# Performance work log

Hardware: AMD Instinct MI355X
Metric: run time of the kernel (lower is better)

## Reference

```python
import jax, jax.numpy as jnp
import numpy as np

B, N, FH, H, FO = 8, 1024, 128, 8, 64
FIN = 2 * FH  # f_hid * 2
NEG = -1e9
SLOPE = 0.2  # leaky_relu negative slope (GAT default)


def setup_inputs() -> dict:
    key = jax.random.key(0)
    ks = jax.random.split(key, 10)
    x = jax.random.normal(ks[0], (B, FIN), jnp.float32)
    A = jax.random.randint(ks[1], (B, N, N), 0, 2, jnp.int32)  # 0/1 dense adjacency
    mask_zero = jnp.ones((B, N, 1), jnp.float32)  # node validity mask
    p_atten = jax.random.uniform(ks[2], (B, N), jnp.float32)  # unused in forward body
    e_atten = jax.random.uniform(ks[3], (B, N, FIN), jnp.float32)
    Npost = jax.random.normal(ks[4], (N, FIN), jnp.float32) * np.float32(1.0 / np.sqrt(FIN))  # kaiming-ish
    w = jax.random.normal(ks[5], (H, FIN, FO), jnp.float32) * np.float32(1.0 / np.sqrt(FIN))
    a_src = jax.random.normal(ks[6], (H, FO), jnp.float32) * np.float32(0.1)
    a_dst = jax.random.normal(ks[7], (H, FO), jnp.float32) * np.float32(0.1)
    bias = jnp.zeros((FO,), jnp.float32)
    return {"x": x, "A": A, "mask_zero": mask_zero, "p_atten": p_atten,
            "e_atten": e_atten, "Npost": Npost, "w": w, "a_src": a_src,
            "a_dst": a_dst, "bias": bias}


def reference(x, A, mask_zero, p_atten, e_atten, Npost, w, a_src, a_dst, bias):
    # broadcast-mul feature gating: x [B,FIN] repeated over N posts, gated by Npost*e_atten
    recx = x[:, None, :] * (Npost[None, :, :] * e_atten)          # [B,N,FIN]
    # BatchGAT (DeepInf-style multi-head graph attention, dropout disabled / eval mode)
    h = jnp.einsum('bnf,hfo->bhno', recx, w)                      # [B,H,N,FO]
    s = jnp.einsum('bhno,ho->bhn', h, a_src)                      # src attention term
    d = jnp.einsum('bhno,ho->bhn', h, a_dst)                      # dst attention term
    logits = jax.nn.leaky_relu(s[:, :, :, None] + d[:, :, None, :], SLOPE)  # [B,H,N,N]
    adj = (A > 0)[:, None, :, :]                                  # [B,1,N,N]
    logits = jnp.where(adj, logits, NEG)
    attn = jax.nn.softmax(logits, axis=-1)                        # masked row softmax
    out = jnp.einsum('bhnm,bhmo->bhno', attn, h) + bias           # aggregate neighbors
    out = out.mean(axis=1)                                        # average heads -> [B,N,FO]
    return out * mask_zero                                        # zero padded nodes
```

## Files before the change

kernel.cpp:

```cpp
#include <hip/hip_runtime.h>

typedef __attribute__((ext_vector_type(8))) short          bf16x8;
typedef __attribute__((ext_vector_type(8))) unsigned short u16x8;
typedef __attribute__((ext_vector_type(4))) unsigned short u16x4;
typedef __attribute__((ext_vector_type(4))) float          f32x4;
typedef __attribute__((ext_vector_type(4))) unsigned int   u32x4;

union U8 { u16x8 u; bf16x8 b; u32x4 w; };
union U4 { u16x4 u; unsigned w[2]; };

__device__ __forceinline__ unsigned short f2bf(float f){
  unsigned u = __float_as_uint(f);
  return (unsigned short)((u + 0x7fffu + ((u >> 16) & 1u)) >> 16);
}
__device__ __forceinline__ unsigned pack_bf16(float lo, float hi){
  unsigned a = __float_as_uint(hi) + 0x8000u;
  unsigned b = __float_as_uint(lo) + 0x8000u;
  return __builtin_amdgcn_perm(a, b, 0x07060302u);
}

#define NN  1024
#define FIN 256
#define NH  8
#define FO  64

__global__ __launch_bounds__(256) void stage0(
    const float* __restrict__ w, const int* __restrict__ A,
    unsigned short* __restrict__ wfrag, unsigned long long* __restrict__ Abits)
{
  const int tid = blockIdx.x * 256 + threadIdx.x;
  if (tid < 16384){
    const int lane = tid & 63, ss = (tid >> 6) & 3, kc = (tid >> 8) & 7, h = tid >> 11;
    const int o = 16 * ss + (lane & 15);
    const int f = kc * 32 + (lane >> 4) * 8;
    u16x8 r;
    #pragma unroll
    for (int j = 0; j < 8; j++) r[j] = f2bf(w[(h * FIN + f + j) * FO + o]);
    *(u16x8*)(wfrag + tid * 8) = r;
  }
  for (int i = tid; i < 8388608; i += 262144){
    unsigned long long m = __ballot(A[i] > 0);
    if ((threadIdx.x & 63) == 0) Abits[i >> 6] = m;
  }
}

__global__ __launch_bounds__(512, 4) void stageA(
    const float* __restrict__ x, const float* __restrict__ e_at,
    const float* __restrict__ Np, const unsigned short* __restrict__ wfrag,
    const float* __restrict__ a_src, const float* __restrict__ a_dst,
    unsigned short* __restrict__ hT,
    float* __restrict__ exps, float* __restrict__ exps2,
    float* __restrict__ expd, float* __restrict__ expd2)
{
  __shared__ unsigned short rex[32 * 264];
  const int t = threadIdx.x;
  const int n0 = blockIdx.x * 32, b = blockIdx.y;

  {
    const int row = t >> 4, f0 = (t & 15) * 16;
    const int nrow = n0 + row;
    const float* ep = e_at + (b * NN + nrow) * FIN + f0;
    const float* qp = Np + nrow * FIN + f0;
    const float* xp = x + b * FIN + f0;
    #pragma unroll
    for (int g = 0; g < 2; g++){
      f32x4 e0 = *(const f32x4*)(ep + g * 8), e1 = *(const f32x4*)(ep + g * 8 + 4);
      f32x4 q0 = *(const f32x4*)(qp + g * 8), q1 = *(const f32x4*)(qp + g * 8 + 4);
      f32x4 x0 = *(const f32x4*)(xp + g * 8), x1 = *(const f32x4*)(xp + g * 8 + 4);
      u16x8 r;
      #pragma unroll
      for (int j = 0; j < 4; j++){
        r[j]     = f2bf(e0[j] * q0[j] * x0[j]);
        r[j + 4] = f2bf(e1[j] * q1[j] * x1[j]);
      }
      *(u16x8*)(rex + row * 264 + f0 + g * 8) = r;
    }
  }
  __syncthreads();

  const int h = t >> 6, lane = t & 63, quad = lane >> 4, l15 = lane & 15;
  const unsigned short* wf = wfrag + h * 16384 + lane * 8;

  f32x4 acc[2][4] = {};
  #pragma unroll
  for (int kc = 0; kc < 8; kc++){
    U8 a0, a1, bf[4];
    a0.u = *(const u16x8*)(rex + l15 * 264 + kc * 32 + quad * 8);
    a1.u = *(const u16x8*)(rex + (16 + l15) * 264 + kc * 32 + quad * 8);
    #pragma unroll
    for (int ss = 0; ss < 4; ss++) bf[ss].u = *(const u16x8*)(wf + (kc * 4 + ss) * 512);
    #pragma unroll
    for (int ss = 0; ss < 4; ss++)
      acc[0][ss] = __builtin_amdgcn_mfma_f32_16x16x32_bf16(a0.b, bf[ss].b, acc[0][ss], 0, 0, 0);
    #pragma unroll
    for (int ss = 0; ss < 4; ss++)
      acc[1][ss] = __builtin_amdgcn_mfma_f32_16x16x32_bf16(a1.b, bf[ss].b, acc[1][ss], 0, 0, 0);
  }

  {
    unsigned short* pan = hT + (size_t)(((b * NH + h) * 32 + (n0 >> 5)) * 64) * 32;
    #pragma unroll
    for (int rg = 0; rg < 2; rg++)
      #pragma unroll
      for (int ss = 0; ss < 4; ss++){
        U4 v;
        v.w[0] = pack_bf16(acc[rg][ss][0], acc[rg][ss][1]);
        v.w[1] = pack_bf16(acc[rg][ss][2], acc[rg][ss][3]);
        *(u16x4*)(pan + (16 * ss + l15) * 32 + rg * 16 + quad * 4) = v.u;
      }
  }

  float as4[4], ad4[4];
  #pragma unroll
  for (int ss = 0; ss < 4; ss++){
    as4[ss] = a_src[h * FO + 16 * ss + l15];
    ad4[ss] = a_dst[h * FO + 16 * ss + l15];
  }
  #pragma unroll
  for (int rg = 0; rg < 2; rg++)
    #pragma unroll
    for (int i = 0; i < 4; i++){
      float ps = 0.f, pd = 0.f;
      #pragma unroll
      for (int ss = 0; ss < 4; ss++){ ps += acc[rg][ss][i] * as4[ss]; pd += acc[rg][ss][i] * ad4[ss]; }
      #pragma unroll
      for (int off = 1; off < 16; off <<= 1){
        ps += __shfl_xor(ps, off);
        pd += __shfl_xor(pd, off);
      }
      if (l15 == 0){
        const int idx = (b * NH + h) * NN + n0 + rg * 16 + quad * 4 + i;
        exps [idx] = __expf(ps);
        exps2[idx] = __expf(0.2f * ps);
        expd [idx] = __expf(pd);
        expd2[idx] = __expf(0.2f * pd);
      }
    }
}

#define PCHUNK(C, PAN)                                                          \
  {                                                                             \
    const int c_ = (C);                                                         \
    const unsigned w0_ = mask_l[l15 * 33 + c_];                                 \
    const unsigned w1_ = mask_l[(16 + l15) * 33 + c_];                          \
    const unsigned ab0_ = w0_ >> (quad * 8), ab1_ = w1_ >> (quad * 8);          \
    f32x4 d0_ = *(const f32x4*)(edh + c_ * 32);                                 \
    f32x4 d1_ = *(const f32x4*)(edh + c_ * 32 + 4);                             \
    f32x4 g0_ = *(const f32x4*)(e2h + c_ * 32);                                 \
    f32x4 g1_ = *(const f32x4*)(e2h + c_ * 32 + 4);                             \
    U8 p0_, p1_;                                                                \
    _Pragma("unroll")                                                           \
    for (int r_ = 0; r_ < 4; r_++){                                             \
      const int j0_ = 2 * r_, j1_ = 2 * r_ + 1;                                 \
      const float dj0_ = (j0_ < 4) ? d0_[j0_] : d1_[j0_ - 4];                   \
      const float gj0_ = (j0_ < 4) ? g0_[j0_] : g1_[j0_ - 4];                   \
      const float dj1_ = (j1_ < 4) ? d0_[j1_] : d1_[j1_ - 4];                   \
      const float gj1_ = (j1_ < 4) ? g0_[j1_] : g1_[j1_ - 4];                   \
      float e00_ = fmaxf(Es0 * dj0_, Es20 * gj0_);                              \
      float e01_ = fmaxf(Es0 * dj1_, Es20 * gj1_);                              \
      float e10_ = fmaxf(Es1 * dj0_, Es21 * gj0_);                              \
      float e11_ = fmaxf(Es1 * dj1_, Es21 * gj1_);                              \
      e00_ = (ab0_ & (1u << j0_)) ? e00_ : 0.f;                                 \
      e01_ = (ab0_ & (1u << j1_)) ? e01_ : 0.f;                                 \
      e10_ = (ab1_ & (1u << j0_)) ? e10_ : 0.f;                                 \
      e11_ = (ab1_ & (1u << j1_)) ? e11_ : 0.f;                                 \
      p0_.w[r_] = pack_bf16(e00_, e01_);                                        \
      p1_.w[r_] = pack_bf16(e10_, e11_);                                        \
    }                                                                           \
    _Pragma("unroll")                                                           \
    for (int ss_ = 0; ss_ < 4; ss_++)                                           \
      acc[0][ss_] = __builtin_amdgcn_mfma_f32_16x16x32_bf16(p0_.b, PAN[ss_].b, acc[0][ss_], 0, 0, 0); \
    accs[0] = __builtin_amdgcn_mfma_f32_16x16x32_bf16(p0_.b, ones.b, accs[0], 0, 0, 0); \
    _Pragma("unroll")                                                           \
    for (int ss_ = 0; ss_ < 4; ss_++)                                           \
      acc[1][ss_] = __builtin_amdgcn_mfma_f32_16x16x32_bf16(p1_.b, PAN[ss_].b, acc[1][ss_], 0, 0, 0); \
    accs[1] = __builtin_amdgcn_mfma_f32_16x16x32_bf16(p1_.b, ones.b, accs[1], 0, 0, 0); \
  }

__global__ __launch_bounds__(1024, 4) void stageB(
    const unsigned* __restrict__ Aw,
    const unsigned short* __restrict__ hT,
    const float* __restrict__ exps, const float* __restrict__ exps2,
    const float* __restrict__ expd, const float* __restrict__ expd2,
    const float* __restrict__ bias, const float* __restrict__ mz,
    float* __restrict__ out)
{
  __shared__ float ed_l[NH * NN];
  __shared__ float e2_l[NH * NN];
  __shared__ unsigned mask_l[32 * 33];
  __shared__ float l_l[NH * 32];
  __shared__ float oacc[32 * 65];
  const int t = threadIdx.x, b = blockIdx.y, n0 = blockIdx.x * 32;
  const int h = (t >> 6) & 7, mh = t >> 9;
  const int lane = t & 63, quad = lane >> 4, l15 = lane & 15;

  for (int i = t; i < 32 * 65; i += 1024) oacc[i] = 0.f;
  if (t < NH * 32) l_l[t] = 0.f;
  {
    const float* s1 = expd  + b * 8192;
    const float* s2 = expd2 + b * 8192;
    *(f32x4*)(ed_l + t * 4)        = *(const f32x4*)(s1 + t * 4);
    *(f32x4*)(ed_l + t * 4 + 4096) = *(const f32x4*)(s1 + t * 4 + 4096);
    *(f32x4*)(e2_l + t * 4)        = *(const f32x4*)(s2 + t * 4);
    *(f32x4*)(e2_l + t * 4 + 4096) = *(const f32x4*)(s2 + t * 4 + 4096);
  }
  mask_l[(t >> 5) * 33 + (t & 31)] = Aw[(b * NN + n0 + (t >> 5)) * 32 + (t & 31)];
  __syncthreads();

  const int hb = (b * NH + h) * NN;
  const float Es0  = exps [hb + n0 + l15],      Es20 = exps2[hb + n0 + l15];
  const float Es1  = exps [hb + n0 + 16 + l15], Es21 = exps2[hb + n0 + 16 + l15];
  const unsigned short* pb = hT + (size_t)(b * NH + h) * 65536 + l15 * 32 + quad * 8;
  const float* edh = ed_l + h * NN + quad * 8;
  const float* e2h = e2_l + h * NN + quad * 8;
  const int c0 = mh * 16;

  U8 ones;
  #pragma unroll
  for (int j = 0; j < 8; j++) ones.u[j] = 0x3F80;

  U8 pan0[4], pan1[4];
  #pragma unroll
  for (int ss = 0; ss < 4; ss++){
    pan0[ss].u = *(const u16x8*)(pb + (size_t)c0 * 2048 + ss * 512);
    pan1[ss].u = *(const u16x8*)(pb + (size_t)(c0 + 1) * 2048 + ss * 512);
  }

  f32x4 acc[2][4] = {};
  f32x4 accs[2] = {};

  for (int cc = 0; cc < 16; cc += 2){
    PCHUNK(c0 + cc, pan0)
    if (cc + 2 < 16){
      #pragma unroll
      for (int ss = 0; ss < 4; ss++)
        pan0[ss].u = *(const u16x8*)(pb + (size_t)(c0 + cc + 2) * 2048 + ss * 512);
    }
    PCHUNK(c0 + cc + 1, pan1)
    if (cc + 3 < 16){
      #pragma unroll
      for (int ss = 0; ss < 4; ss++)
        pan1[ss].u = *(const u16x8*)(pb + (size_t)(c0 + cc + 3) * 2048 + ss * 512);
    }
  }

  if (l15 == 0){
    #pragma unroll
    for (int rg = 0; rg < 2; rg++)
      #pragma unroll
      for (int i = 0; i < 4; i++)
        atomicAdd(&l_l[h * 32 + rg * 16 + quad * 4 + i], accs[rg][i]);
  }
  __syncthreads();

  #pragma unroll
  for (int rg = 0; rg < 2; rg++){
    float inv[4];
    #pragma unroll
    for (int i = 0; i < 4; i++)
      inv[i] = 0.125f / l_l[h * 32 + rg * 16 + quad * 4 + i];
    #pragma unroll
    for (int ss = 0; ss < 4; ss++)
      #pragma unroll
      for (int i = 0; i < 4; i++)
        atomicAdd(&oacc[(rg * 16 + quad * 4 + i) * 65 + ss * 16 + l15], acc[rg][ss][i] * inv[i]);
  }
  __syncthreads();

  for (int i = t; i < 2048; i += 1024){
    const int r = i >> 6, o = i & 63;
    out[(b * NN + n0 + r) * FO + o] = (oacc[r * 65 + o] + bias[o]) * mz[b * NN + n0 + r];
  }
}

extern "C" void kernel_launch(void* const* d_in, const int* in_sizes, int n_in,
                              void* d_out, int out_size, void* d_ws, size_t ws_size,
                              hipStream_t stream)
{
  (void)in_sizes; (void)n_in; (void)out_size; (void)ws_size;
  const float* x    = (const float*)d_in[0];
  const int*   A    = (const int*)d_in[1];
  const float* mz   = (const float*)d_in[2];
  const float* e_at = (const float*)d_in[4];
  const float* Np   = (const float*)d_in[5];
  const float* w    = (const float*)d_in[6];
  const float* asrc = (const float*)d_in[7];
  const float* adst = (const float*)d_in[8];
  const float* bias = (const float*)d_in[9];
  float* out = (float*)d_out;

  char* ws = (char*)d_ws;
  unsigned short* wfrag = (unsigned short*)ws;
  unsigned short* hT    = (unsigned short*)(ws + 262144);
  float* exps  = (float*)(ws + 8650752);
  float* exps2 = (float*)(ws + 8912896);
  float* expd  = (float*)(ws + 9175040);
  float* expd2 = (float*)(ws + 9437184);
  unsigned long long* Abits = (unsigned long long*)(ws + 9699328);

  stage0<<<dim3(1024), dim3(256), 0, stream>>>(w, A, wfrag, Abits);
  stageA<<<dim3(32, 8), dim3(512), 0, stream>>>(x, e_at, Np, wfrag, asrc, adst,
                                                hT, exps, exps2, expd, expd2);
  stageB<<<dim3(32, 8), dim3(1024), 0, stream>>>((const unsigned*)Abits, hT,
                                                 exps, exps2, expd, expd2,
                                                 bias, mz, out);
}
```

Baseline: 177.6 us.

## Split attention stage across head pairs and use global atomics for output

```diff
diff --git a/kernel.cpp b/kernel.cpp
--- a/kernel.cpp
+++ b/kernel.cpp
@@ -26,7 +26,9 @@
 
 __global__ __launch_bounds__(256) void stage0(
     const float* __restrict__ w, const int* __restrict__ A,
-    unsigned short* __restrict__ wfrag, unsigned long long* __restrict__ Abits)
+    const float* __restrict__ bias, const float* __restrict__ mz,
+    unsigned short* __restrict__ wfrag, unsigned long long* __restrict__ Abits,
+    float* __restrict__ out)
 {
   const int tid = blockIdx.x * 256 + threadIdx.x;
   if (tid < 16384){
@@ -37,6 +39,11 @@
     #pragma unroll
     for (int j = 0; j < 8; j++) r[j] = f2bf(w[(h * FIN + f + j) * FO + o]);
     *(u16x8*)(wfrag + tid * 8) = r;
+  }
+  #pragma unroll
+  for (int k = 0; k < 2; k++){
+    const int i = tid + k * 262144;
+    out[i] = bias[i & 63] * mz[i >> 6];
   }
   for (int i = tid; i < 8388608; i += 262144){
     unsigned long long m = __ballot(A[i] > 0);
@@ -52,62 +59,54 @@
     float* __restrict__ exps, float* __restrict__ exps2,
     float* __restrict__ expd, float* __restrict__ expd2)
 {
-  __shared__ unsigned short rex[32 * 264];
+  __shared__ unsigned short rex[16 * 264];
   const int t = threadIdx.x;
-  const int n0 = blockIdx.x * 32, b = blockIdx.y;
+  const int n0 = blockIdx.x * 16, b = blockIdx.y;
 
   {
-    const int row = t >> 4, f0 = (t & 15) * 16;
+    const int row = t >> 5, f0 = (t & 31) * 8;
     const int nrow = n0 + row;
     const float* ep = e_at + (b * NN + nrow) * FIN + f0;
     const float* qp = Np + nrow * FIN + f0;
     const float* xp = x + b * FIN + f0;
-    #pragma unroll
-    for (int g = 0; g < 2; g++){
-      f32x4 e0 = *(const f32x4*)(ep + g * 8), e1 = *(const f32x4*)(ep + g * 8 + 4);
-      f32x4 q0 = *(const f32x4*)(qp + g * 8), q1 = *(const f32x4*)(qp + g * 8 + 4);
-      f32x4 x0 = *(const f32x4*)(xp + g * 8), x1 = *(const f32x4*)(xp + g * 8 + 4);
-      u16x8 r;
-      #pragma unroll
-      for (int j = 0; j < 4; j++){
-        r[j]     = f2bf(e0[j] * q0[j] * x0[j]);
-        r[j + 4] = f2bf(e1[j] * q1[j] * x1[j]);
-      }
-      *(u16x8*)(rex + row * 264 + f0 + g * 8) = r;
-    }
+    f32x4 e0 = *(const f32x4*)ep, e1 = *(const f32x4*)(ep + 4);
+    f32x4 q0 = *(const f32x4*)qp, q1 = *(const f32x4*)(qp + 4);
+    f32x4 x0 = *(const f32x4*)xp, x1 = *(const f32x4*)(xp + 4);
+    u16x8 r;
+    #pragma unroll
+    for (int j = 0; j < 4; j++){
+      r[j]     = f2bf(e0[j] * q0[j] * x0[j]);
+      r[j + 4] = f2bf(e1[j] * q1[j] * x1[j]);
+    }
+    *(u16x8*)(rex + row * 264 + f0) = r;
   }
   __syncthreads();
 
   const int h = t >> 6, lane = t & 63, quad = lane >> 4, l15 = lane & 15;
   const unsigned short* wf = wfrag + h * 16384 + lane * 8;
 
-  f32x4 acc[2][4] = {};
+  f32x4 acc[4] = {};
   #pragma unroll
   for (int kc = 0; kc < 8; kc++){
-    U8 a0, a1, bf[4];
+    U8 a0, bf[4];
     a0.u = *(const u16x8*)(rex + l15 * 264 + kc * 32 + quad * 8);
-    a1.u = *(const u16x8*)(rex + (16 + l15) * 264 + kc * 32 + quad * 8);
     #pragma unroll
     for (int ss = 0; ss < 4; ss++) bf[ss].u = *(const u16x8*)(wf + (kc * 4 + ss) * 512);
     #pragma unroll
     for (int ss = 0; ss < 4; ss++)
-      acc[0][ss] = __builtin_amdgcn_mfma_f32_16x16x32_bf16(a0.b, bf[ss].b, acc[0][ss], 0, 0, 0);
-    #pragma unroll
-    for (int ss = 0; ss < 4; ss++)
-      acc[1][ss] = __builtin_amdgcn_mfma_f32_16x16x32_bf16(a1.b, bf[ss].b, acc[1][ss], 0, 0, 0);
+      acc[ss] = __builtin_amdgcn_mfma_f32_16x16x32_bf16(a0.b, bf[ss].b, acc[ss], 0, 0, 0);
   }
 
   {
-    unsigned short* pan = hT + (size_t)(((b * NH + h) * 32 + (n0 >> 5)) * 64) * 32;
-    #pragma unroll
-    for (int rg = 0; rg < 2; rg++)
-      #pragma unroll
-      for (int ss = 0; ss < 4; ss++){
-        U4 v;
-        v.w[0] = pack_bf16(acc[rg][ss][0], acc[rg][ss][1]);
-        v.w[1] = pack_bf16(acc[rg][ss][2], acc[rg][ss][3]);
-        *(u16x4*)(pan + (16 * ss + l15) * 32 + rg * 16 + quad * 4) = v.u;
-      }
+    const int mtile = blockIdx.x >> 1, moff = (blockIdx.x & 1) * 16;
+    unsigned short* pan = hT + (size_t)(((b * NH + h) * 32 + mtile) * 64) * 32;
+    #pragma unroll
+    for (int ss = 0; ss < 4; ss++){
+      U4 v;
+      v.w[0] = pack_bf16(acc[ss][0], acc[ss][1]);
+      v.w[1] = pack_bf16(acc[ss][2], acc[ss][3]);
+      *(u16x4*)(pan + (16 * ss + l15) * 32 + moff + quad * 4) = v.u;
+    }
   }
 
   float as4[4], ad4[4];
@@ -117,159 +116,115 @@
     ad4[ss] = a_dst[h * FO + 16 * ss + l15];
   }
   #pragma unroll
-  for (int rg = 0; rg < 2; rg++)
-    #pragma unroll
-    for (int i = 0; i < 4; i++){
-      float ps = 0.f, pd = 0.f;
-      #pragma unroll
-      for (int ss = 0; ss < 4; ss++){ ps += acc[rg][ss][i] * as4[ss]; pd += acc[rg][ss][i] * ad4[ss]; }
-      #pragma unroll
-      for (int off = 1; off < 16; off <<= 1){
-        ps += __shfl_xor(ps, off);
-        pd += __shfl_xor(pd, off);
-      }
-      if (l15 == 0){
-        const int idx = (b * NH + h) * NN + n0 + rg * 16 + quad * 4 + i;
-        exps [idx] = __expf(ps);
-        exps2[idx] = __expf(0.2f * ps);
-        expd [idx] = __expf(pd);
-        expd2[idx] = __expf(0.2f * pd);
-      }
-    }
-}
-
-#define PCHUNK(C, PAN)                                                          \
-  {                                                                             \
-    const int c_ = (C);                                                         \
-    const unsigned w0_ = mask_l[l15 * 33 + c_];                                 \
-    const unsigned w1_ = mask_l[(16 + l15) * 33 + c_];                          \
-    const unsigned ab0_ = w0_ >> (quad * 8), ab1_ = w1_ >> (quad * 8);          \
-    f32x4 d0_ = *(const f32x4*)(edh + c_ * 32);                                 \
-    f32x4 d1_ = *(const f32x4*)(edh + c_ * 32 + 4);                             \
-    f32x4 g0_ = *(const f32x4*)(e2h + c_ * 32);                                 \
-    f32x4 g1_ = *(const f32x4*)(e2h + c_ * 32 + 4);                             \
-    U8 p0_, p1_;                                                                \
-    _Pragma("unroll")                                                           \
-    for (int r_ = 0; r_ < 4; r_++){                                             \
-      const int j0_ = 2 * r_, j1_ = 2 * r_ + 1;                                 \
-      const float dj0_ = (j0_ < 4) ? d0_[j0_] : d1_[j0_ - 4];                   \
-      const float gj0_ = (j0_ < 4) ? g0_[j0_] : g1_[j0_ - 4];                   \
-      const float dj1_ = (j1_ < 4) ? d0_[j1_] : d1_[j1_ - 4];                   \
-      const float gj1_ = (j1_ < 4) ? g0_[j1_] : g1_[j1_ - 4];                   \
-      float e00_ = fmaxf(Es0 * dj0_, Es20 * gj0_);                              \
-      float e01_ = fmaxf(Es0 * dj1_, Es20 * gj1_);                              \
-      float e10_ = fmaxf(Es1 * dj0_, Es21 * gj0_);                              \
-      float e11_ = fmaxf(Es1 * dj1_, Es21 * gj1_);                              \
-      e00_ = (ab0_ & (1u << j0_)) ? e00_ : 0.f;                                 \
-      e01_ = (ab0_ & (1u << j1_)) ? e01_ : 0.f;                                 \
-      e10_ = (ab1_ & (1u << j0_)) ? e10_ : 0.f;                                 \
-      e11_ = (ab1_ & (1u << j1_)) ? e11_ : 0.f;                                 \
-      p0_.w[r_] = pack_bf16(e00_, e01_);                                        \
-      p1_.w[r_] = pack_bf16(e10_, e11_);                                        \
-    }                                                                           \
-    _Pragma("unroll")                                                           \
-    for (int ss_ = 0; ss_ < 4; ss_++)                                           \
-      acc[0][ss_] = __builtin_amdgcn_mfma_f32_16x16x32_bf16(p0_.b, PAN[ss_].b, acc[0][ss_], 0, 0, 0); \
-    accs[0] = __builtin_amdgcn_mfma_f32_16x16x32_bf16(p0_.b, ones.b, accs[0], 0, 0, 0); \
-    _Pragma("unroll")                                                           \
-    for (int ss_ = 0; ss_ < 4; ss_++)                                           \
-      acc[1][ss_] = __builtin_amdgcn_mfma_f32_16x16x32_bf16(p1_.b, PAN[ss_].b, acc[1][ss_], 0, 0, 0); \
-    accs[1] = __builtin_amdgcn_mfma_f32_16x16x32_bf16(p1_.b, ones.b, accs[1], 0, 0, 0); \
-  }
-
-__global__ __launch_bounds__(1024, 4) void stageB(
+  for (int i = 0; i < 4; i++){
+    float ps = 0.f, pd = 0.f;
+    #pragma unroll
+    for (int ss = 0; ss < 4; ss++){ ps += acc[ss][i] * as4[ss]; pd += acc[ss][i] * ad4[ss]; }
+    #pragma unroll
+    for (int off = 1; off < 16; off <<= 1){
+      ps += __shfl_xor(ps, off);
+      pd += __shfl_xor(pd, off);
+    }
+    if (l15 == 0){
+      const int idx = (b * NH + h) * NN + n0 + quad * 4 + i;
+      exps [idx] = __expf(ps);
+      exps2[idx] = __expf(0.2f * ps);
+      expd [idx] = __expf(pd);
+      expd2[idx] = __expf(0.2f * pd);
+    }
+  }
+}
+
+__global__ __launch_bounds__(512, 8) void stageB(
     const unsigned* __restrict__ Aw,
     const unsigned short* __restrict__ hT,
     const float* __restrict__ exps, const float* __restrict__ exps2,
     const float* __restrict__ expd, const float* __restrict__ expd2,
-    const float* __restrict__ bias, const float* __restrict__ mz,
-    float* __restrict__ out)
-{
-  __shared__ float ed_l[NH * NN];
-  __shared__ float e2_l[NH * NN];
+    const float* __restrict__ mz, float* __restrict__ out)
+{
+  __shared__ float ed_l[2 * NN];
+  __shared__ float e2_l[2 * NN];
   __shared__ unsigned mask_l[32 * 33];
-  __shared__ float l_l[NH * 32];
-  __shared__ float oacc[32 * 65];
-  const int t = threadIdx.x, b = blockIdx.y, n0 = blockIdx.x * 32;
-  const int h = (t >> 6) & 7, mh = t >> 9;
-  const int lane = t & 63, quad = lane >> 4, l15 = lane & 15;
-
-  for (int i = t; i < 32 * 65; i += 1024) oacc[i] = 0.f;
-  if (t < NH * 32) l_l[t] = 0.f;
+  __shared__ float l_l[4 * 16];
+  const int t = threadIdx.x;
+  const int n0 = blockIdx.x * 32, hq = blockIdx.y, b = blockIdx.z;
+  const int w = t >> 6, lane = t & 63, quad = lane >> 4, l15 = lane & 15;
+  const int hl = w & 1, rg = (w >> 1) & 1, mh = w >> 2;
+  const int h = hq * 2 + hl;
+
+  if (t < 64) l_l[t] = 0.f;
   {
-    const float* s1 = expd  + b * 8192;
-    const float* s2 = expd2 + b * 8192;
-    *(f32x4*)(ed_l + t * 4)        = *(const f32x4*)(s1 + t * 4);
-    *(f32x4*)(ed_l + t * 4 + 4096) = *(const f32x4*)(s1 + t * 4 + 4096);
-    *(f32x4*)(e2_l + t * 4)        = *(const f32x4*)(s2 + t * 4);
-    *(f32x4*)(e2_l + t * 4 + 4096) = *(const f32x4*)(s2 + t * 4 + 4096);
-  }
-  mask_l[(t >> 5) * 33 + (t & 31)] = Aw[(b * NN + n0 + (t >> 5)) * 32 + (t & 31)];
+    const float* s1 = expd  + (b * NH + hq * 2) * NN;
+    const float* s2 = expd2 + (b * NH + hq * 2) * NN;
+    *(f32x4*)(ed_l + t * 4) = *(const f32x4*)(s1 + t * 4);
+    *(f32x4*)(e2_l + t * 4) = *(const f32x4*)(s2 + t * 4);
+  }
+  #pragma unroll
+  for (int k = 0; k < 2; k++){
+    const int i = t + k * 512;
+    mask_l[(i >> 5) * 33 + (i & 31)] = Aw[(b * NN + n0 + (i >> 5)) * 32 + (i & 31)];
+  }
   __syncthreads();
 
   const int hb = (b * NH + h) * NN;
-  const float Es0  = exps [hb + n0 + l15],      Es20 = exps2[hb + n0 + l15];
-  const float Es1  = exps [hb + n0 + 16 + l15], Es21 = exps2[hb + n0 + 16 + l15];
+  const float Es  = exps [hb + n0 + rg * 16 + l15];
+  const float Es2 = exps2[hb + n0 + rg * 16 + l15];
   const unsigned short* pb = hT + (size_t)(b * NH + h) * 65536 + l15 * 32 + quad * 8;
-  const float* edh = ed_l + h * NN + quad * 8;
-  const float* e2h = e2_l + h * NN + quad * 8;
+  const float* edh = ed_l + hl * NN + quad * 8;
+  const float* e2h = e2_l + hl * NN + quad * 8;
+  const unsigned* maskp = mask_l + (rg * 16 + l15) * 33;
   const int c0 = mh * 16;
 
-  U8 ones;
-  #pragma unroll
-  for (int j = 0; j < 8; j++) ones.u[j] = 0x3F80;
-
-  U8 pan0[4], pan1[4];
-  #pragma unroll
-  for (int ss = 0; ss < 4; ss++){
-    pan0[ss].u = *(const u16x8*)(pb + (size_t)c0 * 2048 + ss * 512);
-    pan1[ss].u = *(const u16x8*)(pb + (size_t)(c0 + 1) * 2048 + ss * 512);
-  }
-
-  f32x4 acc[2][4] = {};
-  f32x4 accs[2] = {};
-
-  for (int cc = 0; cc < 16; cc += 2){
-    PCHUNK(c0 + cc, pan0)
-    if (cc + 2 < 16){
+  U8 pan[4];
+  #pragma unroll
+  for (int ss = 0; ss < 4; ss++)
+    pan[ss].u = *(const u16x8*)(pb + (size_t)c0 * 2048 + ss * 512);
+
+  f32x4 acc[4] = {};
+  float lp = 0.f;
+
+  for (int cc = 0; cc < 16; cc++){
+    const int c = c0 + cc;
+    const unsigned am = maskp[c] >> (quad * 8);
+    float pv[8];
+    #pragma unroll
+    for (int g2 = 0; g2 < 2; g2++){
+      f32x4 dv = *(const f32x4*)(edh + c * 32 + g2 * 4);
+      f32x4 gv = *(const f32x4*)(e2h + c * 32 + g2 * 4);
+      #pragma unroll
+      for (int j = 0; j < 4; j++){
+        float e = fmaxf(Es * dv[j], Es2 * gv[j]);
+        pv[g2 * 4 + j] = (am & (1u << (g2 * 4 + j))) ? e : 0.f;
+      }
+    }
+    lp += ((pv[0] + pv[1]) + (pv[2] + pv[3])) + ((pv[4] + pv[5]) + (pv[6] + pv[7]));
+    U8 p;
+    #pragma unroll
+    for (int r = 0; r < 4; r++) p.w[r] = pack_bf16(pv[2 * r], pv[2 * r + 1]);
+    #pragma unroll
+    for (int ss = 0; ss < 4; ss++)
+      acc[ss] = __builtin_amdgcn_mfma_f32_16x16x32_bf16(p.b, pan[ss].b, acc[ss], 0, 0, 0);
+    if (cc + 1 < 16){
       #pragma unroll
       for (int ss = 0; ss < 4; ss++)
-        pan0[ss].u = *(const u16x8*)(pb + (size_t)(c0 + cc + 2) * 2048 + ss * 512);
-    }
-    PCHUNK(c0 + cc + 1, pan1)
-    if (cc + 3 < 16){
-      #pragma unroll
-      for (int ss = 0; ss < 4; ss++)
-        pan1[ss].u = *(const u16x8*)(pb + (size_t)(c0 + cc + 3) * 2048 + ss * 512);
-    }
-  }
-
-  if (l15 == 0){
-    #pragma unroll
-    for (int rg = 0; rg < 2; rg++)
-      #pragma unroll
-      for (int i = 0; i < 4; i++)
-        atomicAdd(&l_l[h * 32 + rg * 16 + quad * 4 + i], accs[rg][i]);
-  }
+        pan[ss].u = *(const u16x8*)(pb + (size_t)(c + 1) * 2048 + ss * 512);
+    }
+  }
+
+  lp += __shfl_xor(lp, 16);
+  lp += __shfl_xor(lp, 32);
+  if (lane < 16) atomicAdd(&l_l[(w & 3) * 16 + lane], lp);
   __syncthreads();
 
-  #pragma unroll
-  for (int rg = 0; rg < 2; rg++){
-    float inv[4];
-    #pragma unroll
-    for (int i = 0; i < 4; i++)
-      inv[i] = 0.125f / l_l[h * 32 + rg * 16 + quad * 4 + i];
+  const float* mzp = mz + b * NN + n0 + rg * 16;
+  #pragma unroll
+  for (int i = 0; i < 4; i++){
+    const int row = quad * 4 + i;
+    const float invm = (0.125f / l_l[(w & 3) * 16 + row]) * mzp[row];
+    float* op = out + (size_t)(b * NN + n0 + rg * 16 + row) * FO + l15;
     #pragma unroll
     for (int ss = 0; ss < 4; ss++)
-      #pragma unroll
-      for (int i = 0; i < 4; i++)
-        atomicAdd(&oacc[(rg * 16 + quad * 4 + i) * 65 + ss * 16 + l15], acc[rg][ss][i] * inv[i]);
-  }
-  __syncthreads();
-
-  for (int i = t; i < 2048; i += 1024){
-    const int r = i >> 6, o = i & 63;
-    out[(b * NN + n0 + r) * FO + o] = (oacc[r * 65 + o] + bias[o]) * mz[b * NN + n0 + r];
+      atomicAdd(op + ss * 16, acc[ss][i] * invm);
   }
 }
 
@@ -298,10 +253,10 @@
   float* expd2 = (float*)(ws + 9437184);
   unsigned long long* Abits = (unsigned long long*)(ws + 9699328);
 
-  stage0<<<dim3(1024), dim3(256), 0, stream>>>(w, A, wfrag, Abits);
-  stageA<<<dim3(32, 8), dim3(512), 0, stream>>>(x, e_at, Np, wfrag, asrc, adst,
+  stage0<<<dim3(1024), dim3(256), 0, stream>>>(w, A, bias, mz, wfrag, Abits, out);
+  stageA<<<dim3(64, 8), dim3(512), 0, stream>>>(x, e_at, Np, wfrag, asrc, adst,
                                                 hT, exps, exps2, expd, expd2);
-  stageB<<<dim3(32, 8), dim3(1024), 0, stream>>>((const unsigned*)Abits, hT,
-                                                 exps, exps2, expd, expd2,
-                                                 bias, mz, out);
-}
+  stageB<<<dim3(32, 4, 8), dim3(512), 0, stream>>>((const unsigned*)Abits, hT,
+                                                   exps, exps2, expd, expd2,
+                                                   mz, out);
+}
```

Result: faster. 170.4 us (-4.1%).
